# Kernel tuning notes

Hardware: AMD Instinct MI355X
Metric: run time of the kernel (lower is better)

Reference implementation:

```python
import jax, jax.numpy as jnp
import numpy as np
import math

TAU = 1.0  # value of the tau buffer (clamped min 0.001 in torch; 1.0 > that)


def setup_inputs() -> dict:
    key = jax.random.key(0)
    k_x, k_g, k_w, k_cb = jax.random.split(key, 4)
    B, n_in, K, E = 65536, 1024, 1024, 256
    x = jax.random.normal(k_x, (B, n_in), dtype=jnp.float32)
    # pre-sampled Gumbel(0,1) noise (torch samples this inside gumbel_softmax)
    u = jax.random.uniform(k_g, (B, K), dtype=jnp.float32, minval=1e-6, maxval=1.0 - 1e-6)
    gumbel = -jnp.log(-jnp.log(u))
    W_enc = jax.random.normal(k_w, (K, n_in), dtype=jnp.float32) / np.sqrt(n_in)
    b_enc = jnp.zeros((K,), dtype=jnp.float32)
    codebook = 0.5 * jax.random.normal(k_cb, (K, E), dtype=jnp.float32)  # init std=0.5
    return {"x": x, "gumbel": gumbel, "W_enc": W_enc, "b_enc": b_enc, "codebook": codebook}


def reference(x, gumbel, W_enc, b_enc, codebook):
    K = W_enc.shape[0]
    logits = x @ W_enc.T + b_enc                      # [B, K]
    soft = jax.nn.softmax((logits + gumbel) / TAU, axis=-1)  # gumbel-softmax, hard=False
    m = jnp.argmax(soft, axis=-1)                     # [B] int
    hard = jax.nn.one_hot(m, K, dtype=soft.dtype)     # [B, K]
    ste = soft + jax.lax.stop_gradient(hard - soft)   # straight-through
    z_q = ste @ codebook                              # [B, E]
    avg_p = soft.mean(axis=0)                         # [K]
    diversity = jnp.sum(avg_p * (jnp.log(jnp.clip(avg_p, 1e-9)) + math.log(K)))
    return (z_q, m, diversity, jnp.zeros((), dtype=z_q.dtype))
```

## Files before the change

kernel.cpp:

```cpp
#include <hip/hip_runtime.h>
#include <math.h>

#define BT 65536
#define NIN 1024
#define KK 1024
#define EE 256
#define MT 32
#define NB 256
#define NCB 4
#define KB 32
#define XS 36
#define WS 260
#define LOGK 6.9314718055994531f

__global__ __launch_bounds__(256, 2)
void vq_main(const float* __restrict__ x, const float* __restrict__ gum,
             const float* __restrict__ W, const float* __restrict__ bias,
             const float* __restrict__ cbk, float* __restrict__ out,
             float* __restrict__ gsum) {
    __shared__ float smem[XS * KB + WS * KB];
    float* xs = smem;
    float* ws = smem + XS * KB;

    const int tid = threadIdx.x;
    const int tc = tid & 31;
    const int tr = tid >> 5;
    const int row0 = blockIdx.x * MT;

    float lg[4][32];
    #pragma unroll
    for (int i = 0; i < 4; ++i)
        #pragma unroll
        for (int t = 0; t < 32; ++t) lg[i][t] = 0.f;

    const int xrow = tid >> 3;
    const int xn   = (tid & 7) << 2;

    for (int kc = 0; kc < NIN / KB; ++kc) {
        const int n0 = kc * KB;
        const float4 xv = *(const float4*)(x + (size_t)(row0 + xrow) * NIN + n0 + xn);
        xs[(xn + 0) * XS + xrow] = xv.x;
        xs[(xn + 1) * XS + xrow] = xv.y;
        xs[(xn + 2) * XS + xrow] = xv.z;
        xs[(xn + 3) * XS + xrow] = xv.w;

        #pragma unroll
        for (int cb = 0; cb < NCB; ++cb) {
            #pragma unroll
            for (int l = 0; l < 8; ++l) {
                const int flat = tid + l * 256;
                const int wn = (flat & 7) << 2;
                const int wc = flat >> 3;
                const float4 wv = *(const float4*)(W + (size_t)(cb * NB + wc) * NIN + n0 + wn);
                ws[(wn + 0) * WS + wc] = wv.x;
                ws[(wn + 1) * WS + wc] = wv.y;
                ws[(wn + 2) * WS + wc] = wv.z;
                ws[(wn + 3) * WS + wc] = wv.w;
            }
            __syncthreads();
            #pragma unroll
            for (int n = 0; n < KB; ++n) {
                const float4 a  = *(const float4*)(xs + n * XS + 4 * tr);
                const float4 b0 = *(const float4*)(ws + n * WS + 8 * tc);
                const float4 b1 = *(const float4*)(ws + n * WS + 8 * tc + 4);
                const float av[4] = {a.x, a.y, a.z, a.w};
                const float bv[8] = {b0.x, b0.y, b0.z, b0.w, b1.x, b1.y, b1.z, b1.w};
                #pragma unroll
                for (int i = 0; i < 4; ++i)
                    #pragma unroll
                    for (int j = 0; j < 8; ++j)
                        lg[i][cb * 8 + j] = fmaf(av[i], bv[j], lg[i][cb * 8 + j]);
            }
            __syncthreads();
        }
    }

    #pragma unroll
    for (int cb = 0; cb < NCB; ++cb) {
        const int cbase = cb * NB + 8 * tc;
        const float4 bb0 = *(const float4*)(bias + cbase);
        const float4 bb1 = *(const float4*)(bias + cbase + 4);
        #pragma unroll
        for (int i = 0; i < 4; ++i) {
            const int row = row0 + 4 * tr + i;
            const float4 g0 = *(const float4*)(gum + (size_t)row * KK + cbase);
            const float4 g1 = *(const float4*)(gum + (size_t)row * KK + cbase + 4);
            lg[i][cb * 8 + 0] += bb0.x + g0.x;
            lg[i][cb * 8 + 1] += bb0.y + g0.y;
            lg[i][cb * 8 + 2] += bb0.z + g0.z;
            lg[i][cb * 8 + 3] += bb0.w + g0.w;
            lg[i][cb * 8 + 4] += bb1.x + g1.x;
            lg[i][cb * 8 + 5] += bb1.y + g1.y;
            lg[i][cb * 8 + 6] += bb1.z + g1.z;
            lg[i][cb * 8 + 7] += bb1.w + g1.w;
        }
    }

    #pragma unroll
    for (int i = 0; i < 4; ++i) {
        float mv = -1e30f; int mi = 0;
        #pragma unroll
        for (int t = 0; t < 32; ++t) {
            const int c = (t >> 3) * NB + 8 * tc + (t & 7);
            if (lg[i][t] > mv) { mv = lg[i][t]; mi = c; }
        }
        #pragma unroll
        for (int off = 1; off < 32; off <<= 1) {
            const float ov = __shfl_xor(mv, off);
            const int   oi = __shfl_xor(mi, off);
            if (ov > mv || (ov == mv && oi < mi)) { mv = ov; mi = oi; }
        }
        float s = 0.f;
        #pragma unroll
        for (int t = 0; t < 32; ++t) {
            const float e = __expf(lg[i][t] - mv);
            lg[i][t] = e;
            s += e;
        }
        #pragma unroll
        for (int off = 1; off < 32; off <<= 1) s += __shfl_xor(s, off);
        const float rinv = 1.f / s;
        #pragma unroll
        for (int t = 0; t < 32; ++t) lg[i][t] *= rinv;

        const int row = row0 + 4 * tr + i;
        const float4 c0 = *(const float4*)(cbk + (size_t)mi * EE + 8 * tc);
        const float4 c1 = *(const float4*)(cbk + (size_t)mi * EE + 8 * tc + 4);
        *(float4*)(out + (size_t)row * EE + 8 * tc)     = c0;
        *(float4*)(out + (size_t)row * EE + 8 * tc + 4) = c1;
        if (tc == 0) out[(size_t)BT * EE + row] = (float)mi;
    }

    #pragma unroll
    for (int t = 0; t < 32; ++t) lg[0][t] += lg[1][t] + lg[2][t] + lg[3][t];
    __syncthreads();
    float* aggp = smem;
    for (int q = tid; q < KK; q += 256) aggp[q] = 0.f;
    __syncthreads();
    #pragma unroll
    for (int t = 0; t < 32; ++t)
        atomicAdd(&aggp[(t >> 3) * NB + 8 * tc + (t & 7)], lg[0][t]);
    __syncthreads();
    for (int q = tid; q < KK; q += 256) atomicAdd(&gsum[q], aggp[q]);
}

__global__ void vq_fin(const float* __restrict__ gsum, float* __restrict__ out) {
    __shared__ float red[4];
    const int tid = threadIdx.x;
    float local = 0.f;
    for (int q = tid; q < KK; q += 256) {
        const float a = gsum[q] * (1.0f / (float)BT);
        local += a * (logf(fmaxf(a, 1e-9f)) + LOGK);
    }
    #pragma unroll
    for (int off = 1; off < 64; off <<= 1) local += __shfl_xor(local, off);
    if ((tid & 63) == 0) red[tid >> 6] = local;
    __syncthreads();
    if (tid == 0) {
        out[(size_t)BT * EE + BT]     = red[0] + red[1] + red[2] + red[3];
        out[(size_t)BT * EE + BT + 1] = 0.f;
    }
}

extern "C" void kernel_launch(void* const* d_in, const int* in_sizes, int n_in,
                              void* d_out, int out_size, void* d_ws, size_t ws_size,
                              hipStream_t stream) {
    const float* x   = (const float*)d_in[0];
    const float* g   = (const float*)d_in[1];
    const float* W   = (const float*)d_in[2];
    const float* b   = (const float*)d_in[3];
    const float* cbk = (const float*)d_in[4];
    float* out  = (float*)d_out;
    float* gsum = (float*)d_ws;

    hipMemsetAsync(gsum, 0, KK * sizeof(float), stream);
    vq_main<<<BT / MT, 256, 0, stream>>>(x, g, W, b, cbk, out, gsum);
    vq_fin<<<1, 256, 0, stream>>>(gsum, out);
}
```

Measured before the change: 2.500 ms.

## Retile logits GEMM so each wavefront owns 8 rows across full K

The thread mapping changes so each 64-lane wavefront computes 8 rows, with each lane holding 16 columns spread across the full 1024-wide K. The whole W tile (16 by 1024) is now staged per k-chunk, which removes the inner codebook-block loop and its extra barriers. Row-wise argmax and softmax reductions now run within a single wavefront via 64-lane shuffles. The cost is a larger shared-memory footprint (about 66KB), which may limit occupancy to one block per CU, plus a narrower k-chunk that means more outer iterations.

```diff
diff --git a/kernel.cpp b/kernel.cpp
--- a/kernel.cpp
+++ b/kernel.cpp
@@ -6,11 +6,9 @@
 #define KK 1024
 #define EE 256
 #define MT 32
-#define NB 256
-#define NCB 4
-#define KB 32
-#define XS 36
-#define WS 260
+#define KB 16
+#define WSP 1028
+#define XSP 16
 #define LOGK 6.9314718055994531f
 
 __global__ __launch_bounds__(256, 2)
@@ -18,128 +16,137 @@
              const float* __restrict__ W, const float* __restrict__ bias,
              const float* __restrict__ cbk, float* __restrict__ out,
              float* __restrict__ gsum) {
-    __shared__ float smem[XS * KB + WS * KB];
+    __shared__ __align__(16) float smem[MT * XSP + KB * WSP];
     float* xs = smem;
-    float* ws = smem + XS * KB;
+    float* ws = smem + MT * XSP;
 
     const int tid = threadIdx.x;
-    const int tc = tid & 31;
-    const int tr = tid >> 5;
+    const int l   = tid & 63;
+    const int wid = tid >> 6;
     const int row0 = blockIdx.x * MT;
 
-    float lg[4][32];
+    float lg[8][16];
     #pragma unroll
-    for (int i = 0; i < 4; ++i)
+    for (int r = 0; r < 8; ++r)
         #pragma unroll
-        for (int t = 0; t < 32; ++t) lg[i][t] = 0.f;
+        for (int t = 0; t < 16; ++t) lg[r][t] = 0.f;
 
-    const int xrow = tid >> 3;
-    const int xn   = (tid & 7) << 2;
+    const int xr = tid >> 2;
+    const int xf = (tid & 3) << 2;
+    const int wc0 = tid >> 2;
+    const int wf  = (tid & 3) << 2;
 
     for (int kc = 0; kc < NIN / KB; ++kc) {
         const int n0 = kc * KB;
-        const float4 xv = *(const float4*)(x + (size_t)(row0 + xrow) * NIN + n0 + xn);
-        xs[(xn + 0) * XS + xrow] = xv.x;
-        xs[(xn + 1) * XS + xrow] = xv.y;
-        xs[(xn + 2) * XS + xrow] = xv.z;
-        xs[(xn + 3) * XS + xrow] = xv.w;
+        if (tid < 128) {
+            const float4 xv = *(const float4*)(x + (size_t)(row0 + xr) * NIN + n0 + xf);
+            *(float4*)(xs + xr * XSP + xf) = xv;
+        }
+        #pragma unroll
+        for (int lw = 0; lw < 16; ++lw) {
+            const int c = wc0 + (lw << 6);
+            const float4 wv = *(const float4*)(W + (size_t)c * NIN + n0 + wf);
+            ws[(wf + 0) * WSP + c] = wv.x;
+            ws[(wf + 1) * WSP + c] = wv.y;
+            ws[(wf + 2) * WSP + c] = wv.z;
+            ws[(wf + 3) * WSP + c] = wv.w;
+        }
+        __syncthreads();
+        #pragma unroll
+        for (int nb = 0; nb < 4; ++nb) {
+            float a4[8][4];
+            #pragma unroll
+            for (int r = 0; r < 8; ++r) {
+                const float4 av = *(const float4*)(xs + (8 * wid + r) * XSP + (nb << 2));
+                a4[r][0] = av.x; a4[r][1] = av.y; a4[r][2] = av.z; a4[r][3] = av.w;
+            }
+            #pragma unroll
+            for (int m = 0; m < 4; ++m) {
+                const int n = (nb << 2) + m;
+                float bf[4][4];
+                #pragma unroll
+                for (int p = 0; p < 4; ++p) {
+                    const float4 bv = *(const float4*)(ws + n * WSP + (p << 8) + (l << 2));
+                    bf[p][0] = bv.x; bf[p][1] = bv.y; bf[p][2] = bv.z; bf[p][3] = bv.w;
+                }
+                #pragma unroll
+                for (int r = 0; r < 8; ++r)
+                    #pragma unroll
+                    for (int p = 0; p < 4; ++p)
+                        #pragma unroll
+                        for (int j = 0; j < 4; ++j)
+                            lg[r][(p << 2) + j] = fmaf(a4[r][m], bf[p][j], lg[r][(p << 2) + j]);
+            }
+        }
+        __syncthreads();
+    }
 
+    float bb[16];
+    #pragma unroll
+    for (int p = 0; p < 4; ++p) {
+        const float4 b4 = *(const float4*)(bias + (p << 8) + (l << 2));
+        bb[(p << 2) + 0] = b4.x; bb[(p << 2) + 1] = b4.y;
+        bb[(p << 2) + 2] = b4.z; bb[(p << 2) + 3] = b4.w;
+    }
+    #pragma unroll
+    for (int r = 0; r < 8; ++r) {
+        const int row = row0 + (wid << 3) + r;
         #pragma unroll
-        for (int cb = 0; cb < NCB; ++cb) {
-            #pragma unroll
-            for (int l = 0; l < 8; ++l) {
-                const int flat = tid + l * 256;
-                const int wn = (flat & 7) << 2;
-                const int wc = flat >> 3;
-                const float4 wv = *(const float4*)(W + (size_t)(cb * NB + wc) * NIN + n0 + wn);
-                ws[(wn + 0) * WS + wc] = wv.x;
-                ws[(wn + 1) * WS + wc] = wv.y;
-                ws[(wn + 2) * WS + wc] = wv.z;
-                ws[(wn + 3) * WS + wc] = wv.w;
-            }
-            __syncthreads();
-            #pragma unroll
-            for (int n = 0; n < KB; ++n) {
-                const float4 a  = *(const float4*)(xs + n * XS + 4 * tr);
-                const float4 b0 = *(const float4*)(ws + n * WS + 8 * tc);
-                const float4 b1 = *(const float4*)(ws + n * WS + 8 * tc + 4);
-                const float av[4] = {a.x, a.y, a.z, a.w};
-                const float bv[8] = {b0.x, b0.y, b0.z, b0.w, b1.x, b1.y, b1.z, b1.w};
-                #pragma unroll
-                for (int i = 0; i < 4; ++i)
-                    #pragma unroll
-                    for (int j = 0; j < 8; ++j)
-                        lg[i][cb * 8 + j] = fmaf(av[i], bv[j], lg[i][cb * 8 + j]);
-            }
-            __syncthreads();
+        for (int p = 0; p < 4; ++p) {
+            const float4 g4 = *(const float4*)(gum + (size_t)row * KK + (p << 8) + (l << 2));
+            lg[r][(p << 2) + 0] += bb[(p << 2) + 0] + g4.x;
+            lg[r][(p << 2) + 1] += bb[(p << 2) + 1] + g4.y;
+            lg[r][(p << 2) + 2] += bb[(p << 2) + 2] + g4.z;
+            lg[r][(p << 2) + 3] += bb[(p << 2) + 3] + g4.w;
         }
     }
 
     #pragma unroll
-    for (int cb = 0; cb < NCB; ++cb) {
-        const int cbase = cb * NB + 8 * tc;
-        const float4 bb0 = *(const float4*)(bias + cbase);
-        const float4 bb1 = *(const float4*)(bias + cbase + 4);
-        #pragma unroll
-        for (int i = 0; i < 4; ++i) {
-            const int row = row0 + 4 * tr + i;
-            const float4 g0 = *(const float4*)(gum + (size_t)row * KK + cbase);
-            const float4 g1 = *(const float4*)(gum + (size_t)row * KK + cbase + 4);
-            lg[i][cb * 8 + 0] += bb0.x + g0.x;
-            lg[i][cb * 8 + 1] += bb0.y + g0.y;
-            lg[i][cb * 8 + 2] += bb0.z + g0.z;
-            lg[i][cb * 8 + 3] += bb0.w + g0.w;
-            lg[i][cb * 8 + 4] += bb1.x + g1.x;
-            lg[i][cb * 8 + 5] += bb1.y + g1.y;
-            lg[i][cb * 8 + 6] += bb1.z + g1.z;
-            lg[i][cb * 8 + 7] += bb1.w + g1.w;
-        }
-    }
-
-    #pragma unroll
-    for (int i = 0; i < 4; ++i) {
+    for (int r = 0; r < 8; ++r) {
         float mv = -1e30f; int mi = 0;
         #pragma unroll
-        for (int t = 0; t < 32; ++t) {
-            const int c = (t >> 3) * NB + 8 * tc + (t & 7);
-            if (lg[i][t] > mv) { mv = lg[i][t]; mi = c; }
+        for (int t = 0; t < 16; ++t) {
+            const int c = ((t >> 2) << 8) + (l << 2) + (t & 3);
+            if (lg[r][t] > mv) { mv = lg[r][t]; mi = c; }
         }
         #pragma unroll
-        for (int off = 1; off < 32; off <<= 1) {
+        for (int off = 1; off < 64; off <<= 1) {
             const float ov = __shfl_xor(mv, off);
             const int   oi = __shfl_xor(mi, off);
             if (ov > mv || (ov == mv && oi < mi)) { mv = ov; mi = oi; }
         }
         float s = 0.f;
         #pragma unroll
-        for (int t = 0; t < 32; ++t) {
-            const float e = __expf(lg[i][t] - mv);
-            lg[i][t] = e;
+        for (int t = 0; t < 16; ++t) {
+            const float e = __expf(lg[r][t] - mv);
+            lg[r][t] = e;
             s += e;
         }
         #pragma unroll
-        for (int off = 1; off < 32; off <<= 1) s += __shfl_xor(s, off);
+        for (int off = 1; off < 64; off <<= 1) s += __shfl_xor(s, off);
         const float rinv = 1.f / s;
         #pragma unroll
-        for (int t = 0; t < 32; ++t) lg[i][t] *= rinv;
+        for (int t = 0; t < 16; ++t) lg[r][t] *= rinv;
 
-        const int row = row0 + 4 * tr + i;
-        const float4 c0 = *(const float4*)(cbk + (size_t)mi * EE + 8 * tc);
-        const float4 c1 = *(const float4*)(cbk + (size_t)mi * EE + 8 * tc + 4);
-        *(float4*)(out + (size_t)row * EE + 8 * tc)     = c0;
-        *(float4*)(out + (size_t)row * EE + 8 * tc + 4) = c1;
-        if (tc == 0) out[(size_t)BT * EE + row] = (float)mi;
+        const int row = row0 + (wid << 3) + r;
+        const float4 cv = *(const float4*)(cbk + (size_t)mi * EE + (l << 2));
+        *(float4*)(out + (size_t)row * EE + (l << 2)) = cv;
+        if (l == 0) out[(size_t)BT * EE + row] = (float)mi;
     }
 
     #pragma unroll
-    for (int t = 0; t < 32; ++t) lg[0][t] += lg[1][t] + lg[2][t] + lg[3][t];
+    for (int t = 0; t < 16; ++t)
+        #pragma unroll
+        for (int r = 1; r < 8; ++r) lg[0][t] += lg[r][t];
     __syncthreads();
     float* aggp = smem;
     for (int q = tid; q < KK; q += 256) aggp[q] = 0.f;
     __syncthreads();
     #pragma unroll
-    for (int t = 0; t < 32; ++t)
-        atomicAdd(&aggp[(t >> 3) * NB + 8 * tc + (t & 7)], lg[0][t]);
+    for (int t = 0; t < 16; ++t) {
+        const int c = ((t >> 2) << 8) + (l << 2) + (t & 3);
+        atomicAdd(&aggp[c], lg[0][t]);
+    }
     __syncthreads();
     for (int q = tid; q < KK; q += 256) atomicAdd(&gsum[q], aggp[q]);
 }
```

Result: slower. 3.612 ms (+44.5%).
